# Kernel tuning notes

Measured on AMD Instinct MI355X. Metric: run time of the kernel, lower is better.

## Reference

```python
import jax, jax.numpy as jnp
import numpy as np

B, N, C, H = 8, 1024, 768, 12
D = C // H  # head_dim = 64
SCALE = D ** -0.5
EPS = 1e-5  # nn.LayerNorm default


def layer_norm(x, gamma, beta):
    # normalize over last dim (head_dim)
    mu = jnp.mean(x, axis=-1, keepdims=True)
    var = jnp.var(x, axis=-1, keepdims=True)
    return (x - mu) * jax.lax.rsqrt(var + EPS) * gamma + beta


def setup_inputs() -> dict:
    key = jax.random.key(0)
    ks = jax.random.split(key, 5)
    s = 0.02
    return {
        "x": jax.random.normal(ks[0], (B, N, C), jnp.float32),
        "qkv_w": jax.random.normal(ks[1], (3 * C, C), jnp.float32) * s,
        "qkv_b": jax.random.normal(ks[2], (3 * C,), jnp.float32) * s,
        "q_gamma": jnp.ones((D,), jnp.float32),
        "q_beta": jnp.zeros((D,), jnp.float32),
        "k_gamma": jnp.ones((D,), jnp.float32),
        "k_beta": jnp.zeros((D,), jnp.float32),
        "proj_w": jax.random.normal(ks[3], (C, C), jnp.float32) * s,
        "proj_b": jax.random.normal(ks[4], (C,), jnp.float32) * s,
    }


def reference(x, qkv_w, qkv_b, q_gamma, q_beta, k_gamma, k_beta, proj_w, proj_b):
    Bx, Nx, Cx = x.shape
    qkv = x @ qkv_w.T + qkv_b                       # [B,N,3C]
    qkv = qkv.reshape(Bx, Nx, 3, H, D).transpose(2, 0, 3, 1, 4)  # [3,B,H,N,D]
    q, k, v = qkv[0], qkv[1], qkv[2]
    q = layer_norm(q, q_gamma, q_beta) * SCALE
    k = layer_norm(k, k_gamma, k_beta)
    attn = jax.nn.softmax(jnp.einsum('bhnd,bhmd->bhnm', q, k), axis=-1)  # [B,H,N,N]
    # attn_drop is identity (p=0, eval)
    out = jnp.einsum('bhnm,bhmd->bhnd', attn, v)    # [B,H,N,D]
    out = out.transpose(0, 2, 1, 3).reshape(Bx, Nx, Cx)
    out = out @ proj_w.T + proj_b                   # proj_drop identity
    return out, attn
```

## Files before the change

kernel.cpp:

```cpp
#include <hip/hip_runtime.h>
#include <hip/hip_bf16.h>
#include <stdint.h>

typedef __bf16 bf16_t;
typedef __bf16 bf16x8 __attribute__((ext_vector_type(8)));
typedef __bf16 bf16x4 __attribute__((ext_vector_type(4)));
typedef float f32x4 __attribute__((ext_vector_type(4)));

#define DEV static __device__ __forceinline__

DEV f32x4 mfma16(bf16x8 a, bf16x8 b, f32x4 c) {
  return __builtin_amdgcn_mfma_f32_16x16x32_bf16(a, b, c, 0, 0, 0);
}

DEV void gll16(const void* g, void* l) {
  __builtin_amdgcn_global_load_lds(
      (const __attribute__((address_space(1))) uint32_t*)g,
      (__attribute__((address_space(3))) uint32_t*)l, 16, 0, 0);
}

DEV int swz128(int row, int c16) {
  return (row << 7) + (((c16 ^ row) & 7) << 4);
}
DEV int swzel128(int row, int col) {
  return (row << 7) + ((((col >> 3) ^ row) & 7) << 4) + ((col & 7) << 1);
}

DEV void stage_tile_gll(const bf16_t* g, long rstride, char* lds, int wave, int lane) {
  int r0 = wave * 8 + (lane >> 3);
  int b = lane & 7;
#pragma unroll
  for (int q = 0; q < 2; q++) {
    int row = q * 32 + r0;
    gll16(g + (long)row * rstride + (((b ^ row) & 7) << 3),
          lds + q * 4096 + wave * 1024);
  }
}

__global__ void __launch_bounds__(256)
cast_all(const float* __restrict__ x, bf16_t* __restrict__ ox,
         const float* __restrict__ w1, bf16_t* __restrict__ ow1,
         const float* __restrict__ w2, bf16_t* __restrict__ ow2) {
  long i = (long)(blockIdx.x * 256 + threadIdx.x) * 8;
  const float* s; bf16_t* d; long off;
  if (i < 6291456L)      { s = x;  d = ox;  off = i; }
  else if (i < 8060928L) { s = w1; d = ow1; off = i - 6291456L; }
  else if (i < 8650752L) { s = w2; d = ow2; off = i - 8060928L; }
  else return;
  float4 a = *(const float4*)(s + off);
  float4 b = *(const float4*)(s + off + 4);
  bf16x8 v;
  v[0] = (bf16_t)a.x; v[1] = (bf16_t)a.y; v[2] = (bf16_t)a.z; v[3] = (bf16_t)a.w;
  v[4] = (bf16_t)b.x; v[5] = (bf16_t)b.y; v[6] = (bf16_t)b.z; v[7] = (bf16_t)b.w;
  *(bf16x8*)(d + off) = v;
}

#define C1Q 0.1803368801111244f

__global__ void __launch_bounds__(256, 2)
gemm_qkv_ln(const bf16_t* __restrict__ A, const bf16_t* __restrict__ Bw,
            const float* __restrict__ bias,
            const float* __restrict__ qg, const float* __restrict__ qb,
            const float* __restrict__ kg, const float* __restrict__ kb,
            bf16_t* __restrict__ qkv, int M, int N, int K) {
  __shared__ __align__(16) char As[16384];
  __shared__ __align__(16) char Bs[16384];
  const int tid = threadIdx.x;
  const int lane = tid & 63;
  const int wave = tid >> 6;
  const int wr = wave >> 1, wc = wave & 1;
  const int tileM = blockIdx.y << 7;
  const int tileN = blockIdx.x << 7;
  const int lrow = lane & 15, lk = lane >> 4;

  f32x4 acc[4][4];
  f32x4 z = {0.f, 0.f, 0.f, 0.f};
#pragma unroll
  for (int m = 0; m < 4; m++)
#pragma unroll
    for (int n = 0; n < 4; n++) acc[m][n] = z;

  for (int k0 = 0; k0 < K; k0 += 64) {
    __syncthreads();
    stage_tile_gll(A + (long)tileM * K + k0, K, As, wave, lane);
    stage_tile_gll(A + (long)(tileM + 64) * K + k0, K, As + 8192, wave, lane);
    stage_tile_gll(Bw + (long)tileN * K + k0, K, Bs, wave, lane);
    stage_tile_gll(Bw + (long)(tileN + 64) * K + k0, K, Bs + 8192, wave, lane);
    __syncthreads();
#pragma unroll
    for (int ks = 0; ks < 2; ks++) {
      bf16x8 af[4], bfr[4];
#pragma unroll
      for (int m = 0; m < 4; m++)
        af[m] = *(const bf16x8*)(As + wr * 8192 + swz128(m * 16 + lrow, ks * 4 + lk));
#pragma unroll
      for (int n = 0; n < 4; n++)
        bfr[n] = *(const bf16x8*)(Bs + wc * 8192 + swz128(n * 16 + lrow, ks * 4 + lk));
#pragma unroll
      for (int m = 0; m < 4; m++)
#pragma unroll
        for (int n = 0; n < 4; n++)
          acc[m][n] = mfma16(af[m], bfr[n], acc[m][n]);
    }
  }

  const int t = tileN / 768;
  const int cbase = tileN + wc * 64;
  float g[4], be[4], bv[4];
#pragma unroll
  for (int n = 0; n < 4; n++) bv[n] = bias[cbase + n * 16 + lrow];
  if (t == 0) {
#pragma unroll
    for (int n = 0; n < 4; n++) {
      int d = n * 16 + lrow;
      g[n] = qg[d] * C1Q; be[n] = qb[d] * C1Q;
    }
  } else if (t == 1) {
#pragma unroll
    for (int n = 0; n < 4; n++) {
      int d = n * 16 + lrow;
      g[n] = kg[d]; be[n] = kb[d];
    }
  }

#pragma unroll
  for (int m = 0; m < 4; m++) {
#pragma unroll
    for (int r = 0; r < 4; r++) {
      float v[4];
#pragma unroll
      for (int n = 0; n < 4; n++) v[n] = acc[m][n][r] + bv[n];
      long row = tileM + wr * 64 + m * 16 + lk * 4 + r;
      bf16_t* dst = qkv + row * 2304 + cbase;
      if (t < 2) {
        float s = v[0] + v[1] + v[2] + v[3];
        float s2 = v[0]*v[0] + v[1]*v[1] + v[2]*v[2] + v[3]*v[3];
#pragma unroll
        for (int ofs = 1; ofs <= 8; ofs <<= 1) {
          s  += __shfl_xor(s, ofs);
          s2 += __shfl_xor(s2, ofs);
        }
        float mu = s * (1.f / 64.f);
        float rstd = rsqrtf(s2 * (1.f / 64.f) - mu * mu + 1e-5f);
#pragma unroll
        for (int n = 0; n < 4; n++)
          dst[n * 16 + lrow] = (bf16_t)((v[n] - mu) * rstd * g[n] + be[n]);
      } else {
#pragma unroll
        for (int n = 0; n < 4; n++)
          dst[n * 16 + lrow] = (bf16_t)v[n];
      }
    }
  }
}

__global__ void __launch_bounds__(256, 2)
gemm_bt(const bf16_t* __restrict__ A, const bf16_t* __restrict__ Bw,
        const float* __restrict__ bias, float* __restrict__ Cout,
        int M, int N, int K) {
  __shared__ __align__(16) char As[16384];
  __shared__ __align__(16) char Bs[16384];
  const int tid = threadIdx.x;
  const int lane = tid & 63;
  const int wave = tid >> 6;
  const int wr = wave >> 1, wc = wave & 1;
  const int tileM = blockIdx.y << 7;
  const int tileN = blockIdx.x << 7;
  const int lrow = lane & 15, lk = lane >> 4;

  f32x4 acc[4][4];
  f32x4 z = {0.f, 0.f, 0.f, 0.f};
#pragma unroll
  for (int m = 0; m < 4; m++)
#pragma unroll
    for (int n = 0; n < 4; n++) acc[m][n] = z;

  for (int k0 = 0; k0 < K; k0 += 64) {
    __syncthreads();
    stage_tile_gll(A + (long)tileM * K + k0, K, As, wave, lane);
    stage_tile_gll(A + (long)(tileM + 64) * K + k0, K, As + 8192, wave, lane);
    stage_tile_gll(Bw + (long)tileN * K + k0, K, Bs, wave, lane);
    stage_tile_gll(Bw + (long)(tileN + 64) * K + k0, K, Bs + 8192, wave, lane);
    __syncthreads();
#pragma unroll
    for (int ks = 0; ks < 2; ks++) {
      bf16x8 af[4], bfr[4];
#pragma unroll
      for (int m = 0; m < 4; m++)
        af[m] = *(const bf16x8*)(As + wr * 8192 + swz128(m * 16 + lrow, ks * 4 + lk));
#pragma unroll
      for (int n = 0; n < 4; n++)
        bfr[n] = *(const bf16x8*)(Bs + wc * 8192 + swz128(n * 16 + lrow, ks * 4 + lk));
#pragma unroll
      for (int m = 0; m < 4; m++)
#pragma unroll
        for (int n = 0; n < 4; n++)
          acc[m][n] = mfma16(af[m], bfr[n], acc[m][n]);
    }
  }

  const int rg = lk;
#pragma unroll
  for (int n = 0; n < 4; n++) {
    int col = tileN + wc * 64 + n * 16 + lrow;
    float bv = bias[col];
#pragma unroll
    for (int m = 0; m < 4; m++) {
      long row0 = tileM + wr * 64 + m * 16 + rg * 4;
#pragma unroll
      for (int r = 0; r < 4; r++)
        Cout[(row0 + r) * N + col] = acc[m][n][r] + bv;
    }
  }
}

__global__ void __launch_bounds__(256, 2)
attn_kernel(const bf16_t* __restrict__ qkv, float* __restrict__ attn_out,
            bf16_t* __restrict__ out_heads) {
  const int tid = threadIdx.x;
  const int lane = tid & 63;
  const int wave = tid >> 6;
  const int lb = blockIdx.x;
  const int sid = (lb & 7) * 192 + (lb >> 3);
  const int qt = sid & 15;
  const int bh = sid >> 4;
  const int b = bh / 12, h = bh - b * 12;

  const bf16_t* base = qkv + (long)b * 2359296L + h * 64;
  const bf16_t* Qg = base;
  const bf16_t* Kg = base + 768;
  const bf16_t* Vg = base + 1536;

  __shared__ __align__(16) char Ks[8192];
  __shared__ __align__(16) char Vt[8192];
  __shared__ __align__(16) char QP[8192];

  const int lrow = lane & 15;
  const int lk = lane >> 4;
  const int sr = tid >> 2;
  const int sc = tid & 3;

  {
    const bf16_t* qp = Qg + (long)(qt * 64 + sr) * 2304 + sc * 8;
    const bf16_t* kp = Kg + (long)sr * 2304 + sc * 8;
    bf16x8 q0 = *(const bf16x8*)(qp);
    bf16x8 q1 = *(const bf16x8*)(qp + 32);
    bf16x8 k0 = *(const bf16x8*)(kp);
    bf16x8 k1 = *(const bf16x8*)(kp + 32);
    *(bf16x8*)(QP + swz128(sr, sc)) = q0;
    *(bf16x8*)(QP + swz128(sr, 4 + sc)) = q1;
    *(bf16x8*)(Ks + swz128(sr, sc)) = k0;
    *(bf16x8*)(Ks + swz128(sr, 4 + sc)) = k1;
  }
  __syncthreads();

  bf16x8 qf[2];
  qf[0] = *(const bf16x8*)(QP + swz128(wave * 16 + lrow, lk));
  qf[1] = *(const bf16x8*)(QP + swz128(wave * 16 + lrow, 4 + lk));

  auto computeS = [&](const char* Kb, f32x4 sfr[4]) {
    f32x4 z = {0.f, 0.f, 0.f, 0.f};
    sfr[0] = z; sfr[1] = z; sfr[2] = z; sfr[3] = z;
#pragma unroll
    for (int kk = 0; kk < 2; kk++)
#pragma unroll
      for (int f = 0; f < 4; f++) {
        bf16x8 kf = *(const bf16x8*)(Kb + swz128(f * 16 + lrow, kk * 4 + lk));
        sfr[f] = mfma16(qf[kk], kf, sfr[f]);
      }
  };

  float l_r[4] = {0.f, 0.f, 0.f, 0.f};

  for (int kt = 0; kt < 16; kt++) {
    const char* cur = (kt & 1) ? Vt : Ks;
    bf16x8 kr0, kr1;
    if (kt < 15) {
      const bf16_t* kp = Kg + (long)((kt + 1) * 64 + sr) * 2304 + sc * 8;
      kr0 = *(const bf16x8*)(kp);
      kr1 = *(const bf16x8*)(kp + 32);
    }
    f32x4 sfr[4];
    computeS(cur, sfr);
#pragma unroll
    for (int r = 0; r < 4; r++)
      l_r[r] += exp2f(sfr[0][r]) + exp2f(sfr[1][r]) +
                exp2f(sfr[2][r]) + exp2f(sfr[3][r]);
    if (kt < 15) {
      char* nxt = (kt & 1) ? Ks : Vt;
      *(bf16x8*)(nxt + swz128(sr, sc)) = kr0;
      *(bf16x8*)(nxt + swz128(sr, 4 + sc)) = kr1;
    }
    __syncthreads();
  }

  float il[4];
#pragma unroll
  for (int r = 0; r < 4; r++) {
#pragma unroll
    for (int ofs = 1; ofs <= 8; ofs <<= 1)
      l_r[r] += __shfl_xor(l_r[r], ofs);
    il[r] = 1.0f / l_r[r];
  }

  f32x4 of[4];
  {
    f32x4 z = {0.f, 0.f, 0.f, 0.f};
    of[0] = z; of[1] = z; of[2] = z; of[3] = z;
  }
  char* Pw = QP + wave * 2048;
  float* attn_base = attn_out + (long)bh * 1048576 + ((long)(qt * 64) << 10);

  const int vk = lane, vdg = wave;
  {
    const bf16_t* kp = Kg + (long)sr * 2304 + sc * 8;
    bf16x8 k0 = *(const bf16x8*)(kp);
    bf16x8 k1 = *(const bf16x8*)(kp + 32);
    const bf16_t* vp = Vg + (long)vk * 2304 + vdg * 16;
    bf16x8 v0 = *(const bf16x8*)(vp);
    bf16x8 v1 = *(const bf16x8*)(vp + 8);
    *(bf16x8*)(Ks + swz128(sr, sc)) = k0;
    *(bf16x8*)(Ks + swz128(sr, 4 + sc)) = k1;
#pragma unroll
    for (int j = 0; j < 8; j++) {
      *(bf16_t*)(Vt + swzel128(vdg * 16 + j, vk)) = v0[j];
      *(bf16_t*)(Vt + swzel128(vdg * 16 + 8 + j, vk)) = v1[j];
    }
  }
  __syncthreads();

  for (int kt = 0; kt < 16; kt++) {
    bf16x8 kr0, kr1, vr0, vr1;
    if (kt < 15) {
      const bf16_t* kp = Kg + (long)((kt + 1) * 64 + sr) * 2304 + sc * 8;
      kr0 = *(const bf16x8*)(kp);
      kr1 = *(const bf16x8*)(kp + 32);
      const bf16_t* vp = Vg + (long)((kt + 1) * 64 + vk) * 2304 + vdg * 16;
      vr0 = *(const bf16x8*)(vp);
      vr1 = *(const bf16x8*)(vp + 8);
    }
    f32x4 sfr[4];
    computeS(Ks, sfr);
#pragma unroll
    for (int f = 0; f < 4; f++)
#pragma unroll
      for (int r = 0; r < 4; r++) {
        float p = exp2f(sfr[f][r]) * il[r];
        *(bf16_t*)(Pw + swzel128(lk * 4 + r, f * 16 + lrow)) = (bf16_t)p;
      }
#pragma unroll
    for (int kk = 0; kk < 2; kk++) {
      bf16x8 pf = *(const bf16x8*)(Pw + swz128(lrow, kk * 4 + lk));
#pragma unroll
      for (int f = 0; f < 4; f++) {
        bf16x8 vf = *(const bf16x8*)(Vt + swz128(f * 16 + lrow, kk * 4 + lk));
        of[f] = mfma16(pf, vf, of[f]);
      }
    }
    float* ab = attn_base + kt * 64;
    {
      const int rsub = lane >> 4;
      const int c8 = lane & 15;
      const char* psrc = Pw + (c8 & 1) * 8;
#pragma unroll
      for (int i = 0; i < 4; i++) {
        int rl = i * 4 + rsub;
        bf16x4 pv = *(const bf16x4*)(psrc + swz128(rl, c8 >> 1));
        f32x4 v = {(float)pv[0], (float)pv[1], (float)pv[2], (float)pv[3]};
        __builtin_nontemporal_store(
            v, (f32x4*)(ab + ((long)(wave * 16 + rl) << 10) + c8 * 4));
      }
    }
    __syncthreads();
    if (kt < 15) {
      *(bf16x8*)(Ks + swz128(sr, sc)) = kr0;
      *(bf16x8*)(Ks + swz128(sr, 4 + sc)) = kr1;
#pragma unroll
      for (int j = 0; j < 8; j++) {
        *(bf16_t*)(Vt + swzel128(vdg * 16 + j, vk)) = vr0[j];
        *(bf16_t*)(Vt + swzel128(vdg * 16 + 8 + j, vk)) = vr1[j];
      }
    }
    __syncthreads();
  }

#pragma unroll
  for (int f = 0; f < 4; f++)
#pragma unroll
    for (int r = 0; r < 4; r++) {
      int nrow = qt * 64 + wave * 16 + lk * 4 + r;
      int d = f * 16 + lrow;
      out_heads[((long)b * 1024 + nrow) * 768 + h * 64 + d] = (bf16_t)of[f][r];
    }
}

extern "C" void kernel_launch(void* const* d_in, const int* in_sizes, int n_in,
                              void* d_out, int out_size, void* d_ws, size_t ws_size,
                              hipStream_t stream) {
  (void)in_sizes; (void)n_in; (void)out_size; (void)ws_size;
  const float* x       = (const float*)d_in[0];
  const float* qkv_w   = (const float*)d_in[1];
  const float* qkv_b   = (const float*)d_in[2];
  const float* q_gamma = (const float*)d_in[3];
  const float* q_beta  = (const float*)d_in[4];
  const float* k_gamma = (const float*)d_in[5];
  const float* k_beta  = (const float*)d_in[6];
  const float* proj_w  = (const float*)d_in[7];
  const float* proj_b  = (const float*)d_in[8];
  float* out = (float*)d_out;

  char* ws = (char*)d_ws;
  bf16_t* x_bf      = (bf16_t*)(ws);
  bf16_t* wqkv      = (bf16_t*)(ws + 12582912L);
  bf16_t* wproj     = (bf16_t*)(ws + 16121856L);
  bf16_t* qkv       = (bf16_t*)(ws + 17301504L);
  bf16_t* out_heads = (bf16_t*)(ws + 55050240L);

  cast_all<<<4224, 256, 0, stream>>>(x, x_bf, qkv_w, wqkv, proj_w, wproj);
  gemm_qkv_ln<<<dim3(18, 64), 256, 0, stream>>>(x_bf, wqkv, qkv_b,
                                                q_gamma, q_beta, k_gamma, k_beta,
                                                qkv, 8192, 2304, 768);
  attn_kernel<<<1536, 256, 0, stream>>>(qkv, out + 6291456L, out_heads);
  gemm_bt<<<dim3(6, 64), 256, 0, stream>>>(out_heads, wproj, proj_b, out, 8192, 768, 768);
}
```

Before: 182.4 us.

## Enlarge attention query tile to 128 rows with 512-thread blocks

Each attention block now has 8 waves and covers 128 query rows instead of 64, so each K/V tile loaded into shared memory is reused by twice as many rows. Per-thread staging work for K and V is halved, and the grid shrinks to 768 blocks. The aim is to cut the redundant global loads of K and V across query tiles. In exchange, each block uses more shared memory, the launch-bounds occupancy hint is dropped, and there are fewer blocks to balance across CUs.

```diff
diff --git a/kernel.cpp b/kernel.cpp
--- a/kernel.cpp
+++ b/kernel.cpp
@@ -214,16 +214,16 @@
   }
 }
 
-__global__ void __launch_bounds__(256, 2)
+__global__ void __launch_bounds__(512)
 attn_kernel(const bf16_t* __restrict__ qkv, float* __restrict__ attn_out,
             bf16_t* __restrict__ out_heads) {
   const int tid = threadIdx.x;
   const int lane = tid & 63;
   const int wave = tid >> 6;
   const int lb = blockIdx.x;
-  const int sid = (lb & 7) * 192 + (lb >> 3);
-  const int qt = sid & 15;
-  const int bh = sid >> 4;
+  const int sid = (lb & 7) * 96 + (lb >> 3);
+  const int qt = sid & 7;
+  const int bh = sid >> 3;
   const int b = bh / 12, h = bh - b * 12;
 
   const bf16_t* base = qkv + (long)b * 2359296L + h * 64;
@@ -231,26 +231,28 @@
   const bf16_t* Kg = base + 768;
   const bf16_t* Vg = base + 1536;
 
+  __shared__ __align__(16) char QP[16384];
   __shared__ __align__(16) char Ks[8192];
   __shared__ __align__(16) char Vt[8192];
-  __shared__ __align__(16) char QP[8192];
 
   const int lrow = lane & 15;
   const int lk = lane >> 4;
-  const int sr = tid >> 2;
-  const int sc = tid & 3;
+  const int qsr = tid >> 2;
+  const int qsc = tid & 3;
+  const int ksr = tid >> 3;
+  const int ksc = tid & 7;
+  const int vk = tid & 63;
+  const int vdg = tid >> 6;
 
   {
-    const bf16_t* qp = Qg + (long)(qt * 64 + sr) * 2304 + sc * 8;
-    const bf16_t* kp = Kg + (long)sr * 2304 + sc * 8;
+    const bf16_t* qp = Qg + (long)(qt * 128 + qsr) * 2304 + qsc * 8;
     bf16x8 q0 = *(const bf16x8*)(qp);
     bf16x8 q1 = *(const bf16x8*)(qp + 32);
+    const bf16_t* kp = Kg + (long)ksr * 2304 + ksc * 8;
     bf16x8 k0 = *(const bf16x8*)(kp);
-    bf16x8 k1 = *(const bf16x8*)(kp + 32);
-    *(bf16x8*)(QP + swz128(sr, sc)) = q0;
-    *(bf16x8*)(QP + swz128(sr, 4 + sc)) = q1;
-    *(bf16x8*)(Ks + swz128(sr, sc)) = k0;
-    *(bf16x8*)(Ks + swz128(sr, 4 + sc)) = k1;
+    *(bf16x8*)(QP + swz128(qsr, qsc)) = q0;
+    *(bf16x8*)(QP + swz128(qsr, 4 + qsc)) = q1;
+    *(bf16x8*)(Ks + swz128(ksr, ksc)) = k0;
   }
   __syncthreads();
 
@@ -274,11 +276,9 @@
 
   for (int kt = 0; kt < 16; kt++) {
     const char* cur = (kt & 1) ? Vt : Ks;
-    bf16x8 kr0, kr1;
+    bf16x8 kr0;
     if (kt < 15) {
-      const bf16_t* kp = Kg + (long)((kt + 1) * 64 + sr) * 2304 + sc * 8;
-      kr0 = *(const bf16x8*)(kp);
-      kr1 = *(const bf16x8*)(kp + 32);
+      kr0 = *(const bf16x8*)(Kg + (long)((kt + 1) * 64 + ksr) * 2304 + ksc * 8);
     }
     f32x4 sfr[4];
     computeS(cur, sfr);
@@ -288,8 +288,7 @@
                 exp2f(sfr[2][r]) + exp2f(sfr[3][r]);
     if (kt < 15) {
       char* nxt = (kt & 1) ? Ks : Vt;
-      *(bf16x8*)(nxt + swz128(sr, sc)) = kr0;
-      *(bf16x8*)(nxt + swz128(sr, 4 + sc)) = kr1;
+      *(bf16x8*)(nxt + swz128(ksr, ksc)) = kr0;
     }
     __syncthreads();
   }
@@ -309,35 +308,25 @@
     of[0] = z; of[1] = z; of[2] = z; of[3] = z;
   }
   char* Pw = QP + wave * 2048;
-  float* attn_base = attn_out + (long)bh * 1048576 + ((long)(qt * 64) << 10);
-
-  const int vk = lane, vdg = wave;
+  float* attn_base = attn_out + (long)bh * 1048576 + ((long)(qt * 128) << 10);
+
   {
-    const bf16_t* kp = Kg + (long)sr * 2304 + sc * 8;
+    const bf16_t* kp = Kg + (long)ksr * 2304 + ksc * 8;
     bf16x8 k0 = *(const bf16x8*)(kp);
-    bf16x8 k1 = *(const bf16x8*)(kp + 32);
-    const bf16_t* vp = Vg + (long)vk * 2304 + vdg * 16;
+    const bf16_t* vp = Vg + (long)vk * 2304 + vdg * 8;
     bf16x8 v0 = *(const bf16x8*)(vp);
-    bf16x8 v1 = *(const bf16x8*)(vp + 8);
-    *(bf16x8*)(Ks + swz128(sr, sc)) = k0;
-    *(bf16x8*)(Ks + swz128(sr, 4 + sc)) = k1;
-#pragma unroll
-    for (int j = 0; j < 8; j++) {
-      *(bf16_t*)(Vt + swzel128(vdg * 16 + j, vk)) = v0[j];
-      *(bf16_t*)(Vt + swzel128(vdg * 16 + 8 + j, vk)) = v1[j];
-    }
+    *(bf16x8*)(Ks + swz128(ksr, ksc)) = k0;
+#pragma unroll
+    for (int j = 0; j < 8; j++)
+      *(bf16_t*)(Vt + swzel128(vdg * 8 + j, vk)) = v0[j];
   }
   __syncthreads();
 
   for (int kt = 0; kt < 16; kt++) {
-    bf16x8 kr0, kr1, vr0, vr1;
+    bf16x8 kr0, vr0;
     if (kt < 15) {
-      const bf16_t* kp = Kg + (long)((kt + 1) * 64 + sr) * 2304 + sc * 8;
-      kr0 = *(const bf16x8*)(kp);
-      kr1 = *(const bf16x8*)(kp + 32);
-      const bf16_t* vp = Vg + (long)((kt + 1) * 64 + vk) * 2304 + vdg * 16;
-      vr0 = *(const bf16x8*)(vp);
-      vr1 = *(const bf16x8*)(vp + 8);
+      kr0 = *(const bf16x8*)(Kg + (long)((kt + 1) * 64 + ksr) * 2304 + ksc * 8);
+      vr0 = *(const bf16x8*)(Vg + (long)((kt + 1) * 64 + vk) * 2304 + vdg * 8);
     }
     f32x4 sfr[4];
     computeS(Ks, sfr);
@@ -373,13 +362,10 @@
     }
     __syncthreads();
     if (kt < 15) {
-      *(bf16x8*)(Ks + swz128(sr, sc)) = kr0;
-      *(bf16x8*)(Ks + swz128(sr, 4 + sc)) = kr1;
-#pragma unroll
-      for (int j = 0; j < 8; j++) {
-        *(bf16_t*)(Vt + swzel128(vdg * 16 + j, vk)) = vr0[j];
-        *(bf16_t*)(Vt + swzel128(vdg * 16 + 8 + j, vk)) = vr1[j];
-      }
+      *(bf16x8*)(Ks + swz128(ksr, ksc)) = kr0;
+#pragma unroll
+      for (int j = 0; j < 8; j++)
+        *(bf16_t*)(Vt + swzel128(vdg * 8 + j, vk)) = vr0[j];
     }
     __syncthreads();
   }
@@ -388,7 +374,7 @@
   for (int f = 0; f < 4; f++)
 #pragma unroll
     for (int r = 0; r < 4; r++) {
-      int nrow = qt * 64 + wave * 16 + lk * 4 + r;
+      int nrow = qt * 128 + wave * 16 + lk * 4 + r;
       int d = f * 16 + lrow;
       out_heads[((long)b * 1024 + nrow) * 768 + h * 64 + d] = (bf16_t)of[f][r];
     }
@@ -420,6 +406,6 @@
   gemm_qkv_ln<<<dim3(18, 64), 256, 0, stream>>>(x_bf, wqkv, qkv_b,
                                                 q_gamma, q_beta, k_gamma, k_beta,
                                                 qkv, 8192, 2304, 768);
-  attn_kernel<<<1536, 256, 0, stream>>>(qkv, out + 6291456L, out_heads);
+  attn_kernel<<<768, 512, 0, stream>>>(qkv, out + 6291456L, out_heads);
   gemm_bt<<<dim3(6, 64), 256, 0, stream>>>(out_heads, wproj, proj_b, out, 8192, 768, 768);
 }
```

Measured after the change: 177.7 us (median of 2 runs). 2.6% less time.
